# Kernel tuning notes

Measured on AMD Instinct MI355X. Metric: run time of the kernel, lower is better.

## Reference

```python
import jax, jax.numpy as jnp
import numpy as np

HIDDEN = 2048
INPUT = 128
BATCH = 2048


def setup_inputs() -> dict:
    key = jax.random.key(0)
    k = jax.random.split(key, 7)
    inp = {
        "input": jax.random.normal(k[0], (BATCH, INPUT), dtype=jnp.float32),
        "hx_real": jax.random.normal(k[1], (BATCH, HIDDEN), dtype=jnp.float32),
        "hx_imag": jax.random.normal(k[2], (BATCH, HIDDEN), dtype=jnp.float32),
        "W_unitary": jax.random.normal(k[3], (5 * HIDDEN, INPUT), dtype=jnp.float32) / np.sqrt(INPUT),
        "b_unitary": jax.random.normal(k[4], (5 * HIDDEN,), dtype=jnp.float32) * 0.01,
        "beta": jnp.zeros((HIDDEN,), dtype=jnp.float32),
        "permutation": jax.random.permutation(k[5], HIDDEN).astype(jnp.int32),
    }
    return inp


def _householder_apply(v, h):
    # (I - 2 v v^H) h = h - 2 v (v^H h); same math as materializing the matrix.
    proj = jnp.sum(jnp.conj(v) * h, axis=-1, keepdims=True)
    return h - 2.0 * v * proj


def reference(input, hx_real, hx_imag, W_unitary, b_unitary, beta, permutation):
    hx = hx_real + 1j * hx_imag  # (B, H) complex64
    up = input @ W_unitary.T + b_unitary  # (B, 5H)
    phases = jnp.exp(1j * up)  # complex64, unit modulus
    d1, d2, d3, r1, r2 = jnp.split(phases, 5, axis=-1)

    h = jnp.fft.fft(d1 * hx, axis=-1)
    h = _householder_apply(r1, h)
    h = jnp.fft.ifft(d2 * h[:, permutation], axis=-1)
    h = d3 * _householder_apply(r2, h)

    # ModReLU: relu(|z| + beta) * exp(1j * angle(z))
    mag = jnp.abs(h)
    new_mag = jax.nn.relu(mag + beta)
    h = new_mag * jnp.exp(1j * jnp.angle(h))
    return h
```

## Files before the change

kernel.cpp:

```cpp
#include <hip/hip_runtime.h>
#include <hip/hip_fp16.h>

#define HID 2048
#define FIVEH 10240
#define INP 128
#define BATCH 2048

typedef _Float16 half8 __attribute__((ext_vector_type(8)));
typedef float f32x4 __attribute__((ext_vector_type(4)));

__device__ __forceinline__ half8 cvt8(const float* p) {
  float4 a = *(const float4*)p;
  float4 b = *(const float4*)(p + 4);
  half8 h;
  h[0] = (_Float16)a.x; h[1] = (_Float16)a.y; h[2] = (_Float16)a.z; h[3] = (_Float16)a.w;
  h[4] = (_Float16)b.x; h[5] = (_Float16)b.y; h[6] = (_Float16)b.z; h[7] = (_Float16)b.w;
  return h;
}

__global__ __launch_bounds__(256) void gemm_up(const float* __restrict__ A,
                                               const float* __restrict__ W,
                                               const float* __restrict__ bias,
                                               _Float16* __restrict__ up16,
                                               int row0, int nrows) {
  int tid = threadIdx.x, wave = tid >> 6, lane = tid & 63;
  int mg_count = nrows >> 6;
  int wid = blockIdx.x * 4 + wave;
  if (wid >= mg_count * 80) return;
  int mg = wid % mg_count;
  int ns = wid / mg_count;
  int nl = lane & 15, quad = lane >> 4;

  half8 af[4][4];
#pragma unroll
  for (int mt = 0; mt < 4; ++mt) {
    const float* arow = A + (size_t)(row0 + mg * 64 + mt * 16 + nl) * INP + quad * 8;
#pragma unroll
    for (int ks = 0; ks < 4; ++ks) af[mt][ks] = cvt8(arow + ks * 32);
  }

#pragma unroll
  for (int nt = 0; nt < 8; ++nt) {
    int ncol = ns * 128 + nt * 16 + nl;
    const float* wrow = W + (size_t)ncol * INP + quad * 8;
    half8 bf[4];
#pragma unroll
    for (int ks = 0; ks < 4; ++ks) bf[ks] = cvt8(wrow + ks * 32);
    float bv = bias[ncol];
#pragma unroll
    for (int mt = 0; mt < 4; ++mt) {
      f32x4 acc = {0.f, 0.f, 0.f, 0.f};
#pragma unroll
      for (int ks = 0; ks < 4; ++ks)
        acc = __builtin_amdgcn_mfma_f32_16x16x32_f16(af[mt][ks], bf[ks], acc, 0, 0, 0);
      int mbase = mg * 64 + mt * 16 + quad * 4;
#pragma unroll
      for (int r = 0; r < 4; ++r)
        up16[(size_t)(mbase + r) * FIVEH + ncol] = (_Float16)(acc[r] + bv);
    }
  }
}

__device__ __forceinline__ float2 h2ld(const __half2* p, int i) {
  return __half22float2(p[i]);
}
__device__ __forceinline__ void h2st(__half2* p, int i, float x, float y) {
  p[i] = __floats2half2_rn(x, y);
}

__device__ __forceinline__ void fft_r4(__half2*& src, __half2*& dst, int tid, float sgn) {
#pragma unroll
  for (int t = 0; t < 4; ++t) {
    int i = tid + (t << 8);
    float2 a = h2ld(src, i), b = h2ld(src, i + 1024);
    h2st(dst, 2 * i,     a.x + b.x, a.y + b.y);
    h2st(dst, 2 * i + 1, a.x - b.x, a.y - b.y);
  }
  __syncthreads();
  { __half2* t = src; src = dst; dst = t; }

#pragma unroll
  for (int pass = 0; pass < 5; ++pass) {
    const int L = 2 << (2 * pass);
    const float co = sgn * 1.5707963267948966f / (float)L;
#pragma unroll
    for (int t = 0; t < 2; ++t) {
      int i = tid + (t << 8);
      int k = i & (L - 1);
      int base4 = ((i - k) << 2) + k;
      float2 x0 = h2ld(src, i),        x1 = h2ld(src, i + 512);
      float2 x2 = h2ld(src, i + 1024), x3 = h2ld(src, i + 1536);
      float ang = co * (float)k;
      float s1, c1; __sincosf(ang, &s1, &c1);
      float c2 = c1 * c1 - s1 * s1, s2 = 2.f * c1 * s1;
      float c3 = c1 * c2 - s1 * s2, s3 = c1 * s2 + s1 * c2;
      float y1r = x1.x * c1 - x1.y * s1, y1i = x1.x * s1 + x1.y * c1;
      float y2r = x2.x * c2 - x2.y * s2, y2i = x2.x * s2 + x2.y * c2;
      float y3r = x3.x * c3 - x3.y * s3, y3i = x3.x * s3 + x3.y * c3;
      float t0r = x0.x + y2r, t0i = x0.y + y2i;
      float t1r = x0.x - y2r, t1i = x0.y - y2i;
      float t2r = y1r + y3r, t2i = y1i + y3i;
      float t3r = y1r - y3r, t3i = y1i - y3i;
      h2st(dst, base4,         t0r + t2r, t0i + t2i);
      h2st(dst, base4 + 2 * L, t0r - t2r, t0i - t2i);
      h2st(dst, base4 + L,     t1r - sgn * t3i, t1i + sgn * t3r);
      h2st(dst, base4 + 3 * L, t1r + sgn * t3i, t1i - sgn * t3r);
    }
    __syncthreads();
    { __half2* t = src; src = dst; dst = t; }
  }
}

__device__ __forceinline__ void block_reduce2(float& pr, float& pi,
                                              float* redr, float* redi, int tid) {
  for (int off = 32; off > 0; off >>= 1) {
    pr += __shfl_down(pr, off, 64);
    pi += __shfl_down(pi, off, 64);
  }
  if ((tid & 63) == 0) { redr[tid >> 6] = pr; redi[tid >> 6] = pi; }
  __syncthreads();
  pr = redr[0] + redr[1] + redr[2] + redr[3];
  pi = redi[0] + redi[1] + redi[2] + redi[3];
  __syncthreads();
}

#define ROW_PIPELINE(UP)                                                        \
  __half2 *ca = sA, *cb = sB;                                                   \
  fft_r4(ca, cb, tid, -1.0f);                                                   \
  float cc[8], ss[8];                                                           \
  {                                                                             \
    float pr = 0.f, pi = 0.f;                                                   \
    _Pragma("unroll") for (int e = 0; e < 8; ++e) {                             \
      int k = tid + (e << 8);                                                   \
      float sv, cv; __sincosf(UP(e, 3), &sv, &cv);                              \
      cc[e] = cv; ss[e] = sv;                                                   \
      float2 h = h2ld(ca, k);                                                   \
      pr += cv * h.x + sv * h.y;                                                \
      pi += cv * h.y - sv * h.x;                                                \
    }                                                                           \
    block_reduce2(pr, pi, redr, redi, tid);                                     \
    _Pragma("unroll") for (int e = 0; e < 8; ++e) {                             \
      int k = tid + (e << 8);                                                   \
      float2 h = h2ld(ca, k);                                                   \
      h2st(ca, k, h.x - 2.f * (cc[e] * pr - ss[e] * pi),                        \
                  h.y - 2.f * (cc[e] * pi + ss[e] * pr));                       \
    }                                                                           \
  }                                                                             \
  __syncthreads();                                                              \
  const float invN = 1.0f / (float)HID;                                         \
  _Pragma("unroll") for (int e = 0; e < 8; ++e) {                               \
    int k = tid + (e << 8);                                                     \
    float sv, cv; __sincosf(UP(e, 1), &sv, &cv);                                \
    float2 h = h2ld(ca, perm[k]);                                               \
    h2st(cb, k, (cv * h.x - sv * h.y) * invN, (cv * h.y + sv * h.x) * invN);    \
  }                                                                             \
  __syncthreads();                                                              \
  { __half2* t = ca; ca = cb; cb = t; }                                         \
  fft_r4(ca, cb, tid, 1.0f);                                                    \
  float prj_r, prj_i;                                                           \
  {                                                                             \
    float pr = 0.f, pi = 0.f;                                                   \
    _Pragma("unroll") for (int e = 0; e < 8; ++e) {                             \
      int k = tid + (e << 8);                                                   \
      float sv, cv; __sincosf(UP(e, 4), &sv, &cv);                              \
      cc[e] = cv; ss[e] = sv;                                                   \
      float2 h = h2ld(ca, k);                                                   \
      pr += cv * h.x + sv * h.y;                                                \
      pi += cv * h.y - sv * h.x;                                                \
    }                                                                           \
    block_reduce2(pr, pi, redr, redi, tid);                                     \
    prj_r = pr; prj_i = pi;                                                     \
  }                                                                             \
  _Pragma("unroll") for (int e = 0; e < 8; ++e) {                               \
    int k = tid + (e << 8);                                                     \
    float2 h = h2ld(ca, k);                                                     \
    float hr = h.x - 2.f * (cc[e] * prj_r - ss[e] * prj_i);                     \
    float hi = h.y - 2.f * (cc[e] * prj_i + ss[e] * prj_r);                     \
    float s3, c3; __sincosf(UP(e, 2), &s3, &c3);                                \
    float zr = c3 * hr - s3 * hi;                                               \
    float zi = c3 * hi + s3 * hr;                                               \
    float mag = sqrtf(zr * zr + zi * zi);                                       \
    float nm = mag + beta[k];                                                   \
    nm = nm > 0.f ? nm : 0.f;                                                   \
    float orr, oii;                                                             \
    if (mag > 0.f) { float sc = nm / mag; orr = zr * sc; oii = zi * sc; }       \
    else { orr = nm; oii = 0.f; }                                               \
    long m = (long)b * HID + k;                                                 \
    if (omode == 1) {                                                           \
      const long half = (long)BATCH * HID;                                      \
      if (half + m < out_size_l) { out[m] = orr; out[half + m] = oii; }         \
    } else if (omode == 0) {                                                    \
      if (2 * m + 1 < out_size_l) {                                             \
        float2 o; o.x = orr; o.y = oii;                                         \
        *(float2*)(out + 2 * m) = o;                                            \
      }                                                                         \
    } else {                                                                    \
      if (m < out_size_l) out[m] = orr;                                         \
    }                                                                           \
  }

__global__ __launch_bounds__(256, 8) void urnn_row(const _Float16* __restrict__ up16,
                                                   const float* __restrict__ hxr,
                                                   const float* __restrict__ hxi,
                                                   const float* __restrict__ beta,
                                                   const int* __restrict__ perm,
                                                   float* __restrict__ out,
                                                   int row0, long out_size_l, int omode) {
  __shared__ __half2 sA[HID], sB[HID];
  __shared__ float redr[4], redi[4];

  int tid = threadIdx.x;
  int b = row0 + blockIdx.x;
  const _Float16* uprow = up16 + (size_t)blockIdx.x * FIVEH;
#define UPG(e, s) ((float)uprow[(s) * HID + tid + ((e) << 8)])

#pragma unroll
  for (int e = 0; e < 8; ++e) {
    int k = tid + (e << 8);
    float sv, cv; __sincosf(UPG(e, 0), &sv, &cv);
    float hr = hxr[(size_t)b * HID + k];
    float hi = hxi[(size_t)b * HID + k];
    h2st(sA, k, cv * hr - sv * hi, cv * hi + sv * hr);
  }
  __syncthreads();
  ROW_PIPELINE(UPG)
#undef UPG
}

__global__ __launch_bounds__(256) void urnn_fused(const float* __restrict__ A,
                                                  const float* __restrict__ W,
                                                  const float* __restrict__ bias,
                                                  const float* __restrict__ hxr,
                                                  const float* __restrict__ hxi,
                                                  const float* __restrict__ beta,
                                                  const int* __restrict__ perm,
                                                  float* __restrict__ out,
                                                  long out_size_l, int omode) {
  __shared__ __half2 sA[HID], sB[HID];
  __shared__ float redr[4], redi[4];
  __shared__ float4 xs4[INP / 4];

  int tid = threadIdx.x;
  int b = blockIdx.x;

  if (tid < INP / 4) xs4[tid] = ((const float4*)(A + (size_t)b * INP))[tid];
  __syncthreads();

  float upreg[40];
#pragma unroll
  for (int se = 0; se < 40; ++se) {
    int n = ((se >> 3) << 11) + ((se & 7) << 8) + tid;
    upreg[se] = bias[n];
  }
  for (int kb = 0; kb < 4; ++kb) {
    float4 xv[8];
#pragma unroll
    for (int j = 0; j < 8; ++j) xv[j] = xs4[kb * 8 + j];
#pragma unroll
    for (int se = 0; se < 40; ++se) {
      int n = ((se >> 3) << 11) + ((se & 7) << 8) + tid;
      const float4* wr = (const float4*)(W + (size_t)n * INP + (kb << 5));
      float a = 0.f;
#pragma unroll
      for (int j = 0; j < 8; ++j) {
        float4 wv = wr[j];
        a += xv[j].x * wv.x + xv[j].y * wv.y + xv[j].z * wv.z + xv[j].w * wv.w;
      }
      upreg[se] += a;
    }
  }
#define UPR(e, s) (upreg[(s) * 8 + (e)])
#pragma unroll
  for (int e = 0; e < 8; ++e) {
    int k = tid + (e << 8);
    float sv, cv; __sincosf(UPR(e, 0), &sv, &cv);
    float hr = hxr[(size_t)b * HID + k];
    float hi = hxi[(size_t)b * HID + k];
    h2st(sA, k, cv * hr - sv * hi, cv * hi + sv * hr);
  }
  __syncthreads();
  ROW_PIPELINE(UPR)
#undef UPR
}

extern "C" void kernel_launch(void* const* d_in, const int* in_sizes, int n_in,
                              void* d_out, int out_size, void* d_ws, size_t ws_size,
                              hipStream_t stream) {
  const float* input   = (const float*)d_in[0];
  const float* hx_real = (const float*)d_in[1];
  const float* hx_imag = (const float*)d_in[2];
  const float* W       = (const float*)d_in[3];
  const float* bvec    = (const float*)d_in[4];
  const float* beta    = (const float*)d_in[5];
  const int*   perm    = (const int*)d_in[6];

  int omode;
  if (out_size == BATCH * HID) omode = 2;
  else if (out_size == 2 * BATCH * HID) omode = 1;
  else omode = 0;

  const size_t rowbytes = (size_t)FIVEH * sizeof(_Float16);
  long chunk = (long)(ws_size / rowbytes);
  if (chunk > BATCH) chunk = BATCH;
  chunk &= ~63L;

  if (chunk >= 64) {
    _Float16* up16 = (_Float16*)d_ws;
    for (long row0 = 0; row0 < BATCH; row0 += chunk) {
      int rows = (int)((row0 + chunk <= BATCH) ? chunk : (BATCH - row0));
      int waves = (rows >> 6) * 80;
      gemm_up<<<(waves + 3) / 4, 256, 0, stream>>>(input, W, bvec, up16, (int)row0, rows);
      urnn_row<<<rows, 256, 0, stream>>>(up16, hx_real, hx_imag, beta, perm,
                                         (float*)d_out, (int)row0, (long)out_size, omode);
    }
  } else {
    urnn_fused<<<BATCH, 256, 0, stream>>>(input, W, bvec, hx_real, hx_imag, beta, perm,
                                          (float*)d_out, (long)out_size, omode);
  }
}
```

Measured before the change: 168.8 us.

## Stage W tile in LDS and coalesce up-projection stores via shared memory

Rewrites the up-projection GEMM to use 2D 128x128 block tiles. Each block converts its 128-column slice of W to fp16 once into LDS, where all four waves share it, so each wave no longer reloads W from global memory. Results are written back through LDS and stored as contiguous 16-byte half8 rows. This replaces the scattered 2-byte strided stores. The trade-off is more LDS use and extra barriers, and the row chunk size must now be a multiple of 128.

```diff
diff --git a/kernel.cpp b/kernel.cpp
--- a/kernel.cpp
+++ b/kernel.cpp
@@ -18,46 +18,75 @@
   return h;
 }
 
+#define WSTRIDE 136
 __global__ __launch_bounds__(256) void gemm_up(const float* __restrict__ A,
                                                const float* __restrict__ W,
                                                const float* __restrict__ bias,
                                                _Float16* __restrict__ up16,
                                                int row0, int nrows) {
+  __shared__ _Float16 Ws[128 * WSTRIDE];
   int tid = threadIdx.x, wave = tid >> 6, lane = tid & 63;
-  int mg_count = nrows >> 6;
-  int wid = blockIdx.x * 4 + wave;
-  if (wid >= mg_count * 80) return;
-  int mg = wid % mg_count;
-  int ns = wid / mg_count;
+  int bx = blockIdx.x;
+  int by = blockIdx.y;
   int nl = lane & 15, quad = lane >> 4;
 
-  half8 af[4][4];
-#pragma unroll
-  for (int mt = 0; mt < 4; ++mt) {
-    const float* arow = A + (size_t)(row0 + mg * 64 + mt * 16 + nl) * INP + quad * 8;
-#pragma unroll
-    for (int ks = 0; ks < 4; ++ks) af[mt][ks] = cvt8(arow + ks * 32);
-  }
-
+  {
+    const float* src = W + (size_t)(bx * 128) * INP;
+#pragma unroll
+    for (int it = 0; it < 8; ++it) {
+      int n = (it * 256 + tid) * 8;
+      int col = n >> 7, k = n & 127;
+      *(half8*)(Ws + col * WSTRIDE + k) = cvt8(src + n);
+    }
+  }
+
+  half8 af[2][4];
+  int rowbase = row0 + by * 128 + wave * 32;
+#pragma unroll
+  for (int mt = 0; mt < 2; ++mt) {
+    const float* ar = A + (size_t)(rowbase + mt * 16 + nl) * INP + quad * 8;
+#pragma unroll
+    for (int ks = 0; ks < 4; ++ks) af[mt][ks] = cvt8(ar + ks * 32);
+  }
+  __syncthreads();
+
+  f32x4 acc[2][8];
 #pragma unroll
   for (int nt = 0; nt < 8; ++nt) {
-    int ncol = ns * 128 + nt * 16 + nl;
-    const float* wrow = W + (size_t)ncol * INP + quad * 8;
     half8 bf[4];
 #pragma unroll
-    for (int ks = 0; ks < 4; ++ks) bf[ks] = cvt8(wrow + ks * 32);
-    float bv = bias[ncol];
-#pragma unroll
-    for (int mt = 0; mt < 4; ++mt) {
-      f32x4 acc = {0.f, 0.f, 0.f, 0.f};
+    for (int ks = 0; ks < 4; ++ks)
+      bf[ks] = *(const half8*)(Ws + (nt * 16 + nl) * WSTRIDE + quad * 8 + ks * 32);
+#pragma unroll
+    for (int mt = 0; mt < 2; ++mt) {
+      f32x4 a = {0.f, 0.f, 0.f, 0.f};
 #pragma unroll
       for (int ks = 0; ks < 4; ++ks)
-        acc = __builtin_amdgcn_mfma_f32_16x16x32_f16(af[mt][ks], bf[ks], acc, 0, 0, 0);
-      int mbase = mg * 64 + mt * 16 + quad * 4;
+        a = __builtin_amdgcn_mfma_f32_16x16x32_f16(af[mt][ks], bf[ks], a, 0, 0, 0);
+      acc[mt][nt] = a;
+    }
+  }
+  __syncthreads();
+
+#pragma unroll
+  for (int nt = 0; nt < 8; ++nt) {
+    float bv = bias[bx * 128 + nt * 16 + nl];
+#pragma unroll
+    for (int mt = 0; mt < 2; ++mt) {
+      int rl = wave * 32 + mt * 16 + quad * 4;
 #pragma unroll
       for (int r = 0; r < 4; ++r)
-        up16[(size_t)(mbase + r) * FIVEH + ncol] = (_Float16)(acc[r] + bv);
-    }
+        Ws[(rl + r) * WSTRIDE + nt * 16 + nl] = (_Float16)(acc[mt][nt][r] + bv);
+    }
+  }
+  __syncthreads();
+
+#pragma unroll
+  for (int it = 0; it < 8; ++it) {
+    int v = it * 256 + tid;
+    int r = v >> 4, c8 = (v & 15) * 8;
+    *(half8*)(up16 + (size_t)(by * 128 + r) * FIVEH + bx * 128 + c8) =
+        *(const half8*)(Ws + r * WSTRIDE + c8);
   }
 }
 
@@ -302,14 +331,14 @@
   const size_t rowbytes = (size_t)FIVEH * sizeof(_Float16);
   long chunk = (long)(ws_size / rowbytes);
   if (chunk > BATCH) chunk = BATCH;
-  chunk &= ~63L;
-
-  if (chunk >= 64) {
+  chunk &= ~127L;
+
+  if (chunk >= 128) {
     _Float16* up16 = (_Float16*)d_ws;
     for (long row0 = 0; row0 < BATCH; row0 += chunk) {
       int rows = (int)((row0 + chunk <= BATCH) ? chunk : (BATCH - row0));
-      int waves = (rows >> 6) * 80;
-      gemm_up<<<(waves + 3) / 4, 256, 0, stream>>>(input, W, bvec, up16, (int)row0, rows);
+      dim3 g(FIVEH / 128, rows / 128);
+      gemm_up<<<g, 256, 0, stream>>>(input, W, bvec, up16, (int)row0, rows);
       urnn_row<<<rows, 256, 0, stream>>>(up16, hx_real, hx_imag, beta, perm,
                                          (float*)d_out, (int)row0, (long)out_size, omode);
     }
```

Measured after the change: 155.0 us. 1.09x faster.
